# Kernel tuning notes

Measured on AMD Instinct MI355X. Metric: run time of the kernel, lower is better.

The kernel has to match this reference:

```python
import jax, jax.numpy as jnp
import numpy as np


def _conv1x1(x, w, b):
    # x: [B,C,H,W], w: [Cout,Cin], b: [Cout]  (1x1 conv == per-pixel linear)
    return jnp.einsum('bchw,oc->bohw', x, w) + b[None, :, None, None]


def setup_inputs() -> dict:
    key = jax.random.key(0)
    ks = jax.random.split(key, 8)
    B, C, H, W = 8, 128, 128, 128
    s = 1.0 / np.sqrt(C)
    return {
        'q_feat': jax.random.normal(ks[0], (B, C, H, W), jnp.float32),
        'kv_feat': jax.random.normal(ks[1], (B, C, H, W), jnp.float32),
        'q_w': jax.random.normal(ks[2], (C, C), jnp.float32) * s,
        'q_b': jax.random.normal(ks[3], (C,), jnp.float32) * 0.01,
        'k_w': jax.random.normal(ks[4], (C, C), jnp.float32) * s,
        'k_b': jax.random.normal(ks[5], (C,), jnp.float32) * 0.01,
        'v_w': jax.random.normal(ks[6], (C, C), jnp.float32) * s,
        'v_b': jax.random.normal(ks[7], (C,), jnp.float32) * 0.01,
    }


def reference(q_feat, kv_feat, q_w, q_b, k_w, k_b, v_w, v_b):
    B, C, H, W = q_feat.shape
    q = _conv1x1(q_feat, q_w, q_b).reshape(B, C, H * W)   # [B,C,N]
    k = _conv1x1(kv_feat, k_w, k_b).reshape(B, C, H * W)  # [B,C,N]
    v = _conv1x1(kv_feat, v_w, v_b).reshape(B, C, H * W)  # [B,C,N]
    k_sm = jax.nn.softmax(k, axis=-1)                     # softmax over spatial dim N
    context = jnp.einsum('bcn,bdn->bcd', v, k_sm)         # [B,C,C]
    out = jnp.einsum('bcd,bdn->bcn', context, q)          # [B,C,N]
    return out.reshape(B, C, H, W)
```

## Files before the change

### kernel.cpp

```cpp
#include <hip/hip_runtime.h>
#include <hip/hip_bf16.h>
#include <cstdint>

#define B_ 8
#define C_ 128
#define N_ 16384
#define CHN 512
#define SN 128
#define NST 4
#define NC (N_ / CHN)
#define SN4 64

typedef __attribute__((ext_vector_type(8))) short short8;
typedef __attribute__((ext_vector_type(4))) float f32x4;
typedef __attribute__((ext_vector_type(4))) unsigned short us4;
typedef unsigned short u16;

__device__ __forceinline__ short f2bf(float f) {
  union { float f; unsigned u; } c; c.f = f;
  unsigned r = (c.u + 0x7FFFu + ((c.u >> 16) & 1u)) >> 16;
  return (short)r;
}

__device__ __forceinline__ unsigned cvtpk(float lo, float hi) {
  unsigned r;
  asm("v_cvt_pk_bf16_f32 %0, %1, %2" : "=v"(r) : "v"(lo), "v"(hi));
  return r;
}

union SB { short8 s8; unsigned u[4]; };

__global__ __launch_bounds__(256) void k0_wcvt(const float* __restrict__ kw,
                                               const float* __restrict__ vw,
                                               u16* __restrict__ wbf) {
  const int g = blockIdx.x * 256 + threadIdx.x;
  const int mat = g >> 12, o4 = g & 4095;
  const float* src = mat ? vw : kw;
  float4 f = reinterpret_cast<const float4*>(src)[o4];
  us4 s;
  s[0] = (u16)f2bf(f.x); s[1] = (u16)f2bf(f.y);
  s[2] = (u16)f2bf(f.z); s[3] = (u16)f2bf(f.w);
  reinterpret_cast<us4*>(wbf + (size_t)mat * C_ * C_)[o4] = s;
}

#define KA_LOADS(ST_) do {                                                   \
  _Pragma("unroll") for (int h_ = 0; h_ < 2; ++h_)                           \
  _Pragma("unroll") for (int j_ = 0; j_ < 16; ++j_)                          \
    xr[h_][j_] = xw[(size_t)j_ * N_ + (ST_) * SN + h_ * 64 + lane];          \
} while (0)

#define KA_XWRITE(BUF_) do {                                                 \
  _Pragma("unroll") for (int h_ = 0; h_ < 2; ++h_) {                         \
    const int n_ = h_ * 64 + lane;                                           \
    unsigned pk_[8];                                                         \
    _Pragma("unroll") for (int p_ = 0; p_ < 8; ++p_)                         \
      pk_[p_] = cvtpk(xr[h_][2 * p_], xr[h_][2 * p_ + 1]);                   \
    _Pragma("unroll") for (int o_ = 0; o_ < 2; ++o_) {                       \
      uint4 q_;                                                              \
      q_.x = pk_[o_ * 4]; q_.y = pk_[o_ * 4 + 1];                            \
      q_.z = pk_[o_ * 4 + 2]; q_.w = pk_[o_ * 4 + 3];                        \
      *reinterpret_cast<uint4*>(                                             \
          (BUF_) + n_ * SN + ((w * 16 + o_ * 8) ^ ((n_ & 7) << 3))) = q_;    \
    }                                                                        \
  }                                                                          \
} while (0)

__global__ __launch_bounds__(512, 2) void ka_projctx(
    const float* __restrict__ kv, const u16* __restrict__ wbf,
    const float* __restrict__ kb, const float* __restrict__ vb,
    float* __restrict__ part, float* __restrict__ zpart) {
  __shared__ u16 xt[2][C_ * SN];
  __shared__ u16 eks[C_ * SN];
  __shared__ u16 vs [C_ * SN];

  const int b = blockIdx.y, kc = blockIdx.x;
  const int tid = threadIdx.x;
  const int w = tid >> 6, lane = tid & 63;
  const int lg = lane >> 4, li = lane & 15;
  const int mat = w >> 2, dblk = w & 3;
  const int cg = w >> 1, dh = w & 1;

  const float* xb = kv + (size_t)b * C_ * N_ + (size_t)kc * CHN;
  const float* xw = xb + (size_t)(w * 16) * N_;
  const u16* Wm = wbf + (size_t)mat * C_ * C_;
  const float* biasp = mat ? vb : kb;
  u16* S = mat ? vs : eks;

  short8 wreg[2][4];
#pragma unroll
  for (int dt = 0; dt < 2; ++dt)
#pragma unroll
    for (int ks = 0; ks < 4; ++ks)
      wreg[dt][ks] = *reinterpret_cast<const short8*>(
          Wm + (dblk * 32 + dt * 16 + li) * C_ + ks * 32 + lg * 8);
  float bias2[2];
#pragma unroll
  for (int dt = 0; dt < 2; ++dt) bias2[dt] = biasp[dblk * 32 + dt * 16 + li];

  f32x4 acc[2][4] = {};
  float zac[2] = {0.f, 0.f};
  float xr[2][16];

  KA_LOADS(0);
  KA_XWRITE(&xt[0][0]);
  KA_LOADS(1);
  asm volatile("s_waitcnt lgkmcnt(0)" ::: "memory");
  __builtin_amdgcn_s_barrier();
  __builtin_amdgcn_sched_barrier(0);

#pragma unroll
  for (int st = 0; st < NST; ++st) {
    const u16* xc = &xt[st & 1][0];

    if (st < NST - 1) {
      KA_XWRITE(&xt[(st + 1) & 1][0]);
      if (st < NST - 2) KA_LOADS(st + 2);
    }

#pragma unroll
    for (int h2 = 0; h2 < 4; ++h2) {
      f32x4 pacc[2][2] = {};
#pragma unroll
      for (int ntl = 0; ntl < 2; ++ntl) {
        const int n = (h2 * 2 + ntl) * 16 + li;
#pragma unroll
        for (int ks = 0; ks < 4; ++ks) {
          short8 a = *reinterpret_cast<const short8*>(
              xc + n * SN + ((ks * 32 + lg * 8) ^ ((n & 7) << 3)));
#pragma unroll
          for (int dt = 0; dt < 2; ++dt)
            pacc[ntl][dt] = __builtin_amdgcn_mfma_f32_16x16x32_bf16(
                a, wreg[dt][ks], pacc[ntl][dt], 0, 0, 0);
        }
      }
#pragma unroll
      for (int dt = 0; dt < 2; ++dt) {
        const int d = dblk * 32 + dt * 16 + li;
        const float bias = bias2[dt];
#pragma unroll
        for (int ntl = 0; ntl < 2; ++ntl) {
          float v0 = pacc[ntl][dt][0] + bias;
          float v1 = pacc[ntl][dt][1] + bias;
          float v2 = pacc[ntl][dt][2] + bias;
          float v3 = pacc[ntl][dt][3] + bias;
          if (mat == 0) {
            v0 = __expf(v0); v1 = __expf(v1); v2 = __expf(v2); v3 = __expf(v3);
            zac[dt] += (v0 + v1) + (v2 + v3);
          }
          const int nq = (h2 * 2 + ntl) * 16 + lg * 4;
          uint2 pk; pk.x = cvtpk(v0, v1); pk.y = cvtpk(v2, v3);
          *reinterpret_cast<uint2*>(S + d * SN + (nq ^ ((d & 7) << 3))) = pk;
        }
      }
    }
    asm volatile("s_waitcnt lgkmcnt(0)" ::: "memory");
    __builtin_amdgcn_s_barrier();
    __builtin_amdgcn_sched_barrier(0);

#pragma unroll
    for (int kk = 0; kk < 4; ++kk) {
      const int n0 = kk * 32 + lg * 8;
      short8 a[2], bb[4];
#pragma unroll
      for (int am = 0; am < 2; ++am) {
        const int c = cg * 32 + am * 16 + li;
        a[am] = *reinterpret_cast<const short8*>(vs + c * SN + (n0 ^ ((c & 7) << 3)));
      }
#pragma unroll
      for (int dt = 0; dt < 4; ++dt) {
        const int d = dh * 64 + dt * 16 + li;
        bb[dt] = *reinterpret_cast<const short8*>(eks + d * SN + (n0 ^ ((d & 7) << 3)));
      }
#pragma unroll
      for (int am = 0; am < 2; ++am)
#pragma unroll
        for (int dt = 0; dt < 4; ++dt)
          acc[am][dt] = __builtin_amdgcn_mfma_f32_16x16x32_bf16(a[am], bb[dt], acc[am][dt], 0, 0, 0);
    }
    asm volatile("s_waitcnt lgkmcnt(0)" ::: "memory");
    __builtin_amdgcn_s_barrier();
    __builtin_amdgcn_sched_barrier(0);
  }

  float* P = part + ((size_t)kc * B_ + b) * C_ * C_;
#pragma unroll
  for (int am = 0; am < 2; ++am)
#pragma unroll
    for (int dt = 0; dt < 4; ++dt)
#pragma unroll
      for (int r = 0; r < 4; ++r) {
        const int c = cg * 32 + am * 16 + lg * 4 + r;
        const int d = dh * 64 + dt * 16 + li;
        P[c * C_ + d] = acc[am][dt][r];
      }
  if (mat == 0) {
#pragma unroll
    for (int dt = 0; dt < 2; ++dt) {
      float z = zac[dt];
      z += __shfl_xor(z, 16);
      z += __shfl_xor(z, 32);
      if (lg == 0)
        zpart[((size_t)kc * B_ + b) * C_ + dblk * 32 + dt * 16 + li] = z;
    }
  }
}

__global__ __launch_bounds__(256) void kb2_fin(
    const float* __restrict__ part, const float* __restrict__ zpart,
    const float* __restrict__ qw, const float* __restrict__ qb,
    u16* __restrict__ M, float* __restrict__ T) {
  const int b = blockIdx.y;
  const int cs0 = blockIdx.x * 16;
  const int tid = threadIdx.x;
  __shared__ float cs[16][128];
  __shared__ float Zs[128];
  if (tid < 128) {
    float s = 0.f;
    for (int kc = 0; kc < NC; ++kc)
      s += zpart[((size_t)kc * B_ + b) * C_ + tid];
    Zs[tid] = s;
  }
  __syncthreads();
#pragma unroll
  for (int i = 0; i < 8; ++i) {
    const int e = tid + i * 256;
    const int cl = e >> 7, d = e & 127;
    float s = 0.f;
    for (int kc = 0; kc < NC; ++kc)
      s += part[(((size_t)kc * B_ + b) * C_ + (cs0 + cl)) * C_ + d];
    cs[cl][d] = s / Zs[d];
  }
  __syncthreads();
  const int cl = tid >> 4, e0 = (tid & 15) * 8;
  float m[8] = {};
  for (int d = 0; d < 128; ++d) {
    const float cv = cs[cl][d];
    const float* qr = qw + d * C_ + e0;
#pragma unroll
    for (int j = 0; j < 8; ++j) m[j] += cv * qr[j];
  }
  u16* mp = M + ((size_t)b * C_ + cs0 + cl) * C_ + e0;
#pragma unroll
  for (int j = 0; j < 8; ++j) mp[j] = (u16)f2bf(m[j]);
  if (tid < 16) {
    float tv = 0.f;
    for (int d = 0; d < 128; ++d) tv += cs[tid][d] * qb[d];
    T[b * C_ + cs0 + tid] = tv;
  }
}

__global__ __launch_bounds__(256) void k4_out(const u16* __restrict__ M,
                                              const float* __restrict__ T,
                                              const float* __restrict__ q,
                                              float* __restrict__ out) {
  __shared__ u16 qt[SN4 * C_];
  const int b = blockIdx.y;
  const int n0 = blockIdx.x * SN4;
  const int tid = threadIdx.x;
  const int w = tid >> 6, lane = tid & 63;
  const int lg = lane >> 4, li = lane & 15;

  const float* qb = q + (size_t)b * C_ * N_ + n0;
  float xr[32];
#pragma unroll
  for (int j = 0; j < 32; ++j)
    xr[j] = qb[(size_t)(w * 32 + j) * N_ + lane];

  short8 mreg[2][4];
  const u16* Mb = M + (size_t)b * C_ * C_;
#pragma unroll
  for (int ct = 0; ct < 2; ++ct)
#pragma unroll
    for (int ks = 0; ks < 4; ++ks)
      mreg[ct][ks] = *reinterpret_cast<const short8*>(
          Mb + (w * 32 + ct * 16 + li) * C_ + ks * 32 + lg * 8);
  float tcv[2][4];
#pragma unroll
  for (int ct = 0; ct < 2; ++ct)
#pragma unroll
    for (int r = 0; r < 4; ++r)
      tcv[ct][r] = T[b * C_ + w * 32 + ct * 16 + lg * 4 + r];

#pragma unroll
  for (int o = 0; o < 4; ++o) {
    uint4 v;
    v.x = cvtpk(xr[o * 8 + 0], xr[o * 8 + 1]);
    v.y = cvtpk(xr[o * 8 + 2], xr[o * 8 + 3]);
    v.z = cvtpk(xr[o * 8 + 4], xr[o * 8 + 5]);
    v.w = cvtpk(xr[o * 8 + 6], xr[o * 8 + 7]);
    *reinterpret_cast<uint4*>(
        qt + lane * C_ + ((w * 32 + o * 8) ^ ((lane & 7) << 3))) = v;
  }
  __syncthreads();

  f32x4 acc[2][4] = {};
#pragma unroll
  for (int nt = 0; nt < 4; ++nt) {
    const int n = nt * 16 + li;
#pragma unroll
    for (int ks = 0; ks < 4; ++ks) {
      short8 bb = *reinterpret_cast<const short8*>(
          qt + n * C_ + ((ks * 32 + lg * 8) ^ ((n & 7) << 3)));
#pragma unroll
      for (int ct = 0; ct < 2; ++ct)
        acc[ct][nt] = __builtin_amdgcn_mfma_f32_16x16x32_bf16(
            mreg[ct][ks], bb, acc[ct][nt], 0, 0, 0);
    }
  }

#pragma unroll
  for (int ct = 0; ct < 2; ++ct)
#pragma unroll
    for (int r = 0; r < 4; ++r) {
      const int c = w * 32 + ct * 16 + lg * 4 + r;
      float* op = out + ((size_t)b * C_ + c) * N_ + n0;
      const float t = tcv[ct][r];
#pragma unroll
      for (int nt = 0; nt < 4; ++nt)
        op[nt * 16 + li] = acc[ct][nt][r] + t;
    }
}

extern "C" void kernel_launch(void* const* d_in, const int* in_sizes, int n_in,
                              void* d_out, int out_size, void* d_ws, size_t ws_size,
                              hipStream_t stream) {
  const float* q_feat  = (const float*)d_in[0];
  const float* kv_feat = (const float*)d_in[1];
  const float* q_w = (const float*)d_in[2];
  const float* q_b = (const float*)d_in[3];
  const float* k_w = (const float*)d_in[4];
  const float* k_b = (const float*)d_in[5];
  const float* v_w = (const float*)d_in[6];
  const float* v_b = (const float*)d_in[7];
  float* out = (float*)d_out;

  char* ws = (char*)d_ws;
  const size_t szPart = (size_t)NC * B_ * C_ * C_ * sizeof(float);
  const size_t szZp   = (size_t)NC * B_ * C_ * sizeof(float);
  const size_t szWbf  = (size_t)2 * C_ * C_ * sizeof(u16);
  const size_t szM    = (size_t)B_ * C_ * C_ * sizeof(u16);

  float* part  = (float*)ws;
  float* zpart = (float*)(ws + szPart);
  u16*   wbf   = (u16*)(ws + szPart + szZp);
  u16*   M     = (u16*)(ws + szPart + szZp + szWbf);
  float* T     = (float*)(ws + szPart + szZp + szWbf + szM);

  k0_wcvt<<<dim3(32), 256, 0, stream>>>(k_w, v_w, wbf);
  ka_projctx<<<dim3(NC, B_), 512, 0, stream>>>(kv_feat, wbf, k_b, v_b, part, zpart);
  kb2_fin<<<dim3(8, B_), 256, 0, stream>>>(part, zpart, q_w, q_b, M, T);
  k4_out<<<dim3(N_ / SN4, B_), 256, 0, stream>>>(M, T, q_feat, out);
}
```

Baseline: 75.80 us.

## Process two spatial tiles per block in k4_out with prefetched loads

The output kernel now handles 128 spatial positions per block as two 64-wide tiles. The second tile's global loads are issued before the first tile's MFMA work, into a double-buffered LDS tile, so load latency overlaps compute. The M and T register loads are also amortized over twice the work. The cost is more registers, twice the LDS per block and half as many blocks, which may lower occupancy.

```diff
diff --git a/kernel.cpp b/kernel.cpp
--- a/kernel.cpp
+++ b/kernel.cpp
@@ -249,22 +249,57 @@
   }
 }
 
+#define K4_LOADS(DST_, NOFF_) do {                                           \
+  _Pragma("unroll") for (int j_ = 0; j_ < 32; ++j_)                          \
+    DST_[j_] = qb[(size_t)(w * 32 + j_) * N_ + (NOFF_) + lane];              \
+} while (0)
+
+#define K4_XWRITE(BUF_, SRC_) do {                                           \
+  _Pragma("unroll") for (int o_ = 0; o_ < 4; ++o_) {                         \
+    uint4 v_;                                                                \
+    v_.x = cvtpk(SRC_[o_ * 8 + 0], SRC_[o_ * 8 + 1]);                        \
+    v_.y = cvtpk(SRC_[o_ * 8 + 2], SRC_[o_ * 8 + 3]);                        \
+    v_.z = cvtpk(SRC_[o_ * 8 + 4], SRC_[o_ * 8 + 5]);                        \
+    v_.w = cvtpk(SRC_[o_ * 8 + 6], SRC_[o_ * 8 + 7]);                        \
+    *reinterpret_cast<uint4*>(                                               \
+        (BUF_) + lane * C_ + ((w * 32 + o_ * 8) ^ ((lane & 7) << 3))) = v_;  \
+  }                                                                          \
+} while (0)
+
+#define K4_MFMA_STORE(BUF_, NOFF_) do {                                      \
+  f32x4 acc_[2][4] = {};                                                     \
+  _Pragma("unroll") for (int nt_ = 0; nt_ < 4; ++nt_) {                      \
+    const int n_ = nt_ * 16 + li;                                            \
+    _Pragma("unroll") for (int ks_ = 0; ks_ < 4; ++ks_) {                    \
+      short8 bb_ = *reinterpret_cast<const short8*>(                         \
+          (BUF_) + n_ * C_ + ((ks_ * 32 + lg * 8) ^ ((n_ & 7) << 3)));       \
+      _Pragma("unroll") for (int ct_ = 0; ct_ < 2; ++ct_)                    \
+        acc_[ct_][nt_] = __builtin_amdgcn_mfma_f32_16x16x32_bf16(            \
+            mreg[ct_][ks_], bb_, acc_[ct_][nt_], 0, 0, 0);                   \
+    }                                                                        \
+  }                                                                          \
+  _Pragma("unroll") for (int ct_ = 0; ct_ < 2; ++ct_)                        \
+  _Pragma("unroll") for (int r_ = 0; r_ < 4; ++r_) {                         \
+    const int c_ = w * 32 + ct_ * 16 + lg * 4 + r_;                          \
+    float* op_ = out + ((size_t)b * C_ + c_) * N_ + nb + (NOFF_);            \
+    const float t_ = tcv[ct_][r_];                                           \
+    _Pragma("unroll") for (int nt_ = 0; nt_ < 4; ++nt_)                      \
+      op_[nt_ * 16 + li] = acc_[ct_][nt_][r_] + t_;                          \
+  }                                                                          \
+} while (0)
+
 __global__ __launch_bounds__(256) void k4_out(const u16* __restrict__ M,
                                               const float* __restrict__ T,
                                               const float* __restrict__ q,
                                               float* __restrict__ out) {
-  __shared__ u16 qt[SN4 * C_];
+  __shared__ u16 qt[2][SN4 * C_];
   const int b = blockIdx.y;
-  const int n0 = blockIdx.x * SN4;
+  const int nb = blockIdx.x * 128;
   const int tid = threadIdx.x;
   const int w = tid >> 6, lane = tid & 63;
   const int lg = lane >> 4, li = lane & 15;
 
-  const float* qb = q + (size_t)b * C_ * N_ + n0;
-  float xr[32];
-#pragma unroll
-  for (int j = 0; j < 32; ++j)
-    xr[j] = qb[(size_t)(w * 32 + j) * N_ + lane];
+  const float* qb = q + (size_t)b * C_ * N_ + nb;
 
   short8 mreg[2][4];
   const u16* Mb = M + (size_t)b * C_ * C_;
@@ -281,44 +316,22 @@
     for (int r = 0; r < 4; ++r)
       tcv[ct][r] = T[b * C_ + w * 32 + ct * 16 + lg * 4 + r];
 
-#pragma unroll
-  for (int o = 0; o < 4; ++o) {
-    uint4 v;
-    v.x = cvtpk(xr[o * 8 + 0], xr[o * 8 + 1]);
-    v.y = cvtpk(xr[o * 8 + 2], xr[o * 8 + 3]);
-    v.z = cvtpk(xr[o * 8 + 4], xr[o * 8 + 5]);
-    v.w = cvtpk(xr[o * 8 + 6], xr[o * 8 + 7]);
-    *reinterpret_cast<uint4*>(
-        qt + lane * C_ + ((w * 32 + o * 8) ^ ((lane & 7) << 3))) = v;
-  }
-  __syncthreads();
-
-  f32x4 acc[2][4] = {};
-#pragma unroll
-  for (int nt = 0; nt < 4; ++nt) {
-    const int n = nt * 16 + li;
-#pragma unroll
-    for (int ks = 0; ks < 4; ++ks) {
-      short8 bb = *reinterpret_cast<const short8*>(
-          qt + n * C_ + ((ks * 32 + lg * 8) ^ ((n & 7) << 3)));
-#pragma unroll
-      for (int ct = 0; ct < 2; ++ct)
-        acc[ct][nt] = __builtin_amdgcn_mfma_f32_16x16x32_bf16(
-            mreg[ct][ks], bb, acc[ct][nt], 0, 0, 0);
-    }
-  }
-
-#pragma unroll
-  for (int ct = 0; ct < 2; ++ct)
-#pragma unroll
-    for (int r = 0; r < 4; ++r) {
-      const int c = w * 32 + ct * 16 + lg * 4 + r;
-      float* op = out + ((size_t)b * C_ + c) * N_ + n0;
-      const float t = tcv[ct][r];
-#pragma unroll
-      for (int nt = 0; nt < 4; ++nt)
-        op[nt * 16 + li] = acc[ct][nt][r] + t;
-    }
+  float xr0[32], xr1[32];
+  K4_LOADS(xr0, 0);
+  K4_XWRITE(&qt[0][0], xr0);
+  K4_LOADS(xr1, SN4);
+  asm volatile("s_waitcnt lgkmcnt(0)" ::: "memory");
+  __builtin_amdgcn_s_barrier();
+  __builtin_amdgcn_sched_barrier(0);
+
+  K4_MFMA_STORE(&qt[0][0], 0);
+
+  K4_XWRITE(&qt[1][0], xr1);
+  asm volatile("s_waitcnt lgkmcnt(0)" ::: "memory");
+  __builtin_amdgcn_s_barrier();
+  __builtin_amdgcn_sched_barrier(0);
+
+  K4_MFMA_STORE(&qt[1][0], SN4);
 }
 
 extern "C" void kernel_launch(void* const* d_in, const int* in_sizes, int n_in,
@@ -349,5 +362,5 @@
   k0_wcvt<<<dim3(32), 256, 0, stream>>>(k_w, v_w, wbf);
   ka_projctx<<<dim3(NC, B_), 512, 0, stream>>>(kv_feat, wbf, k_b, v_b, part, zpart);
   kb2_fin<<<dim3(8, B_), 256, 0, stream>>>(part, zpart, q_w, q_b, M, T);
-  k4_out<<<dim3(N_ / SN4, B_), 256, 0, stream>>>(M, T, q_feat, out);
-}
+  k4_out<<<dim3(N_ / 128, B_), 256, 0, stream>>>(M, T, q_feat, out);
+}
```

Result: no change. 75.73 us (-0.1%).

## Restructure output kernel into persistent double-buffered pipeline with swizzled block mapping

Applied to the files above, without the earlier changes.

The output GEMM kernel changes from many small 64-column blocks of 256 threads to 256 blocks of 512 threads. Each block walks a 512-column chunk in four 128-column stages, with double-buffered LDS so global loads and bf16 conversion of the next stage overlap MFMA work on the current one. Both the projection/context kernel and the output kernel also remap block IDs so consecutive blocks span different batches, which may spread memory traffic across channels. The cost is far fewer blocks (256 on the device), so latency hiding now depends on the in-block pipeline, and each block uses more LDS and registers.

```diff
diff --git a/kernel.cpp b/kernel.cpp
--- a/kernel.cpp
+++ b/kernel.cpp
@@ -9,7 +9,6 @@
 #define SN 128
 #define NST 4
 #define NC (N_ / CHN)
-#define SN4 64
 
 typedef __attribute__((ext_vector_type(8))) short short8;
 typedef __attribute__((ext_vector_type(4))) float f32x4;
@@ -73,7 +72,9 @@
   __shared__ u16 eks[C_ * SN];
   __shared__ u16 vs [C_ * SN];
 
-  const int b = blockIdx.y, kc = blockIdx.x;
+  const int fid = blockIdx.x + blockIdx.y * NC;
+  const int fid2 = (fid & 7) * 32 + (fid >> 3);
+  const int b = fid2 >> 5, kc = fid2 & 31;
   const int tid = threadIdx.x;
   const int w = tid >> 6, lane = tid & 63;
   const int lg = lane >> 4, li = lane & 15;
@@ -249,76 +250,99 @@
   }
 }
 
-__global__ __launch_bounds__(256) void k4_out(const u16* __restrict__ M,
+#define K4_LOADS(ST_) do {                                                   \
+  _Pragma("unroll") for (int h_ = 0; h_ < 2; ++h_)                           \
+  _Pragma("unroll") for (int j_ = 0; j_ < 16; ++j_)                          \
+    xr[h_][j_] = qw_[(size_t)j_ * N_ + (ST_) * SN + h_ * 64 + lane];         \
+} while (0)
+
+#define K4_XWRITE(BUF_) do {                                                 \
+  _Pragma("unroll") for (int h_ = 0; h_ < 2; ++h_) {                         \
+    const int n_ = h_ * 64 + lane;                                           \
+    unsigned pk_[8];                                                         \
+    _Pragma("unroll") for (int p_ = 0; p_ < 8; ++p_)                         \
+      pk_[p_] = cvtpk(xr[h_][2 * p_], xr[h_][2 * p_ + 1]);                   \
+    _Pragma("unroll") for (int o_ = 0; o_ < 2; ++o_) {                       \
+      uint4 q_;                                                              \
+      q_.x = pk_[o_ * 4]; q_.y = pk_[o_ * 4 + 1];                            \
+      q_.z = pk_[o_ * 4 + 2]; q_.w = pk_[o_ * 4 + 3];                        \
+      *reinterpret_cast<uint4*>(                                             \
+          (BUF_) + n_ * SN + ((w * 16 + o_ * 8) ^ ((n_ & 7) << 3))) = q_;    \
+    }                                                                        \
+  }                                                                          \
+} while (0)
+
+__global__ __launch_bounds__(512) void k4_out(const u16* __restrict__ M,
                                               const float* __restrict__ T,
                                               const float* __restrict__ q,
                                               float* __restrict__ out) {
-  __shared__ u16 qt[SN4 * C_];
-  const int b = blockIdx.y;
-  const int n0 = blockIdx.x * SN4;
+  __shared__ u16 qt[2][SN * C_];
+
+  const int fid = blockIdx.x + blockIdx.y * NC;
+  const int fid2 = (fid & 7) * 32 + (fid >> 3);
+  const int b = fid2 >> 5, kc = fid2 & 31;
+  const int nb = kc * CHN;
   const int tid = threadIdx.x;
   const int w = tid >> 6, lane = tid & 63;
   const int lg = lane >> 4, li = lane & 15;
 
-  const float* qb = q + (size_t)b * C_ * N_ + n0;
-  float xr[32];
-#pragma unroll
-  for (int j = 0; j < 32; ++j)
-    xr[j] = qb[(size_t)(w * 32 + j) * N_ + lane];
-
-  short8 mreg[2][4];
+  const float* qw_ = q + (size_t)b * C_ * N_ + nb + (size_t)(w * 16) * N_;
+
+  short8 mreg[4];
   const u16* Mb = M + (size_t)b * C_ * C_;
 #pragma unroll
-  for (int ct = 0; ct < 2; ++ct)
-#pragma unroll
-    for (int ks = 0; ks < 4; ++ks)
-      mreg[ct][ks] = *reinterpret_cast<const short8*>(
-          Mb + (w * 32 + ct * 16 + li) * C_ + ks * 32 + lg * 8);
-  float tcv[2][4];
-#pragma unroll
-  for (int ct = 0; ct < 2; ++ct)
-#pragma unroll
-    for (int r = 0; r < 4; ++r)
-      tcv[ct][r] = T[b * C_ + w * 32 + ct * 16 + lg * 4 + r];
-
-#pragma unroll
-  for (int o = 0; o < 4; ++o) {
-    uint4 v;
-    v.x = cvtpk(xr[o * 8 + 0], xr[o * 8 + 1]);
-    v.y = cvtpk(xr[o * 8 + 2], xr[o * 8 + 3]);
-    v.z = cvtpk(xr[o * 8 + 4], xr[o * 8 + 5]);
-    v.w = cvtpk(xr[o * 8 + 6], xr[o * 8 + 7]);
-    *reinterpret_cast<uint4*>(
-        qt + lane * C_ + ((w * 32 + o * 8) ^ ((lane & 7) << 3))) = v;
-  }
-  __syncthreads();
-
-  f32x4 acc[2][4] = {};
-#pragma unroll
-  for (int nt = 0; nt < 4; ++nt) {
-    const int n = nt * 16 + li;
-#pragma unroll
-    for (int ks = 0; ks < 4; ++ks) {
-      short8 bb = *reinterpret_cast<const short8*>(
-          qt + n * C_ + ((ks * 32 + lg * 8) ^ ((n & 7) << 3)));
-#pragma unroll
-      for (int ct = 0; ct < 2; ++ct)
-        acc[ct][nt] = __builtin_amdgcn_mfma_f32_16x16x32_bf16(
-            mreg[ct][ks], bb, acc[ct][nt], 0, 0, 0);
-    }
-  }
-
-#pragma unroll
-  for (int ct = 0; ct < 2; ++ct)
+  for (int ks = 0; ks < 4; ++ks)
+    mreg[ks] = *reinterpret_cast<const short8*>(
+        Mb + (w * 16 + li) * C_ + ks * 32 + lg * 8);
+  float tcv[4];
+#pragma unroll
+  for (int r = 0; r < 4; ++r) tcv[r] = T[b * C_ + w * 16 + lg * 4 + r];
+
+  float xr[2][16];
+
+  K4_LOADS(0);
+  K4_XWRITE(&qt[0][0]);
+  K4_LOADS(1);
+  asm volatile("s_waitcnt lgkmcnt(0)" ::: "memory");
+  __builtin_amdgcn_s_barrier();
+  __builtin_amdgcn_sched_barrier(0);
+
+#pragma unroll
+  for (int st = 0; st < NST; ++st) {
+    const u16* xc = &qt[st & 1][0];
+
+    if (st < NST - 1) {
+      K4_XWRITE(&qt[(st + 1) & 1][0]);
+      if (st < NST - 2) K4_LOADS(st + 2);
+    }
+
+    f32x4 acc[8] = {};
+#pragma unroll
+    for (int nt = 0; nt < 8; ++nt) {
+      const int n = nt * 16 + li;
+#pragma unroll
+      for (int ks = 0; ks < 4; ++ks) {
+        short8 bb = *reinterpret_cast<const short8*>(
+            xc + n * SN + ((ks * 32 + lg * 8) ^ ((n & 7) << 3)));
+        acc[nt] = __builtin_amdgcn_mfma_f32_16x16x32_bf16(
+            mreg[ks], bb, acc[nt], 0, 0, 0);
+      }
+    }
+
 #pragma unroll
     for (int r = 0; r < 4; ++r) {
-      const int c = w * 32 + ct * 16 + lg * 4 + r;
-      float* op = out + ((size_t)b * C_ + c) * N_ + n0;
-      const float t = tcv[ct][r];
-#pragma unroll
-      for (int nt = 0; nt < 4; ++nt)
-        op[nt * 16 + li] = acc[ct][nt][r] + t;
-    }
+      const int c = w * 16 + lg * 4 + r;
+      float* op = out + ((size_t)b * C_ + c) * N_ + nb + st * SN;
+      const float t = tcv[r];
+#pragma unroll
+      for (int nt = 0; nt < 8; ++nt)
+        op[nt * 16 + li] = acc[nt][r] + t;
+    }
+
+    asm volatile("s_waitcnt lgkmcnt(0)" ::: "memory");
+    __builtin_amdgcn_s_barrier();
+    __builtin_amdgcn_sched_barrier(0);
+  }
 }
 
 extern "C" void kernel_launch(void* const* d_in, const int* in_sizes, int n_in,
@@ -349,5 +373,5 @@
   k0_wcvt<<<dim3(32), 256, 0, stream>>>(k_w, v_w, wbf);
   ka_projctx<<<dim3(NC, B_), 512, 0, stream>>>(kv_feat, wbf, k_b, v_b, part, zpart);
   kb2_fin<<<dim3(8, B_), 256, 0, stream>>>(part, zpart, q_w, q_b, M, T);
-  k4_out<<<dim3(N_ / SN4, B_), 256, 0, stream>>>(M, T, q_feat, out);
-}
+  k4_out<<<dim3(NC, B_), 512, 0, stream>>>(M, T, q_feat, out);
+}
```

Result: faster. 73.22 us (-3.4%).
